# Performance work log

Measured on AMD Instinct MI355X. Metric: run time of the kernel, lower is better.

The kernel has to match this reference:

```python
import jax, jax.numpy as jnp
import numpy as np

EPS = 1e-5
K = 20
NEG_SLOPE = 0.2


def lrelu(x):
    return jnp.where(x >= 0, x, NEG_SLOPE * x)


def bn_train(x, w, b, axes):
    # training-mode batch norm (biased variance), channel axis = 1
    m = jnp.mean(x, axis=axes, keepdims=True)
    v = jnp.mean((x - m) ** 2, axis=axes, keepdims=True)
    shp = [1] * x.ndim
    shp[1] = -1
    return (x - m) * jax.lax.rsqrt(v + EPS) * w.reshape(shp) + b.reshape(shp)


def knn_idx(x, k):
    # x: [B, C, N] -> idx [B, N, k] of k nearest neighbors (max of -dist^2)
    inner = -2.0 * jnp.einsum('bcn,bcm->bnm', x, x)
    xx = jnp.sum(x * x, axis=1)  # [B, N]
    pd = -xx[:, None, :] - inner - xx[:, :, None]  # [B, N, N]
    return jax.lax.top_k(pd, k)[1]


def graph_feature(x, k):
    # x: [B, C, N] -> [B, 2C, N, k] = cat(neighbor - center, center)
    B = x.shape[0]
    idx = knn_idx(x, k)  # [B, N, k]
    xt = jnp.transpose(x, (0, 2, 1))  # [B, N, C]
    nbr = xt[jnp.arange(B)[:, None, None], idx]  # [B, N, k, C] gather
    ctr = jnp.broadcast_to(xt[:, :, None, :], nbr.shape)
    feat = jnp.concatenate([nbr - ctr, ctr], axis=-1)  # [B, N, k, 2C]
    return jnp.transpose(feat, (0, 3, 1, 2))


def edge_conv(x, w, bw, bb):
    # EdgeConv: graph feature -> 1x1 conv (no bias) -> BN -> LeakyReLU -> max over k
    f = graph_feature(x, K)                      # [B, 2C, N, k]
    y = jnp.einsum('bcnk,oc->bonk', f, w)        # 1x1 conv2d
    y = lrelu(bn_train(y, bw, bb, (0, 2, 3)))
    return jnp.max(y, axis=-1)                   # [B, O, N]


def setup_inputs() -> dict:
    key = jax.random.key(0)
    ks = jax.random.split(key, 12)
    B, N = 8, 1024
    s = 0.05
    inp = {'x': jax.random.normal(ks[0], (B, 3, N), dtype=jnp.float32)}
    inp['c1w'] = jax.random.normal(ks[1], (64, 6), dtype=jnp.float32) * s
    inp['c2w'] = jax.random.normal(ks[2], (64, 128), dtype=jnp.float32) * s
    inp['c3w'] = jax.random.normal(ks[3], (128, 128), dtype=jnp.float32) * s
    inp['c4w'] = jax.random.normal(ks[4], (256, 256), dtype=jnp.float32) * s
    inp['c5w'] = jax.random.normal(ks[5], (1024, 512), dtype=jnp.float32) * s
    for i, c in zip(range(1, 8), [64, 64, 128, 256, 1024, 512, 256]):
        inp[f'b{i}w'] = jnp.ones((c,), dtype=jnp.float32)
        inp[f'b{i}b'] = jnp.zeros((c,), dtype=jnp.float32)
    inp['l1w'] = jax.random.normal(ks[6], (512, 2048), dtype=jnp.float32) * s
    inp['l1b'] = jnp.zeros((512,), dtype=jnp.float32)
    inp['l2w'] = jax.random.normal(ks[7], (256, 512), dtype=jnp.float32) * s
    inp['l2b'] = jnp.zeros((256,), dtype=jnp.float32)
    inp['l3w'] = jax.random.normal(ks[8], (40, 256), dtype=jnp.float32) * s
    inp['l3b'] = jnp.zeros((40,), dtype=jnp.float32)
    return inp


def reference(x, c1w, c2w, c3w, c4w, c5w,
              b1w, b1b, b2w, b2b, b3w, b3b, b4w, b4b, b5w, b5b,
              b6w, b6b, b7w, b7b,
              l1w, l1b, l2w, l2b, l3w, l3b):
    x1 = edge_conv(x, c1w, b1w, b1b)    # [B, 64, N]
    x2 = edge_conv(x1, c2w, b2w, b2b)   # [B, 64, N]
    x3 = edge_conv(x2, c3w, b3w, b3b)   # [B, 128, N]
    x4 = edge_conv(x3, c4w, b4w, b4b)   # [B, 256, N]
    cat = jnp.concatenate([x1, x2, x3, x4], axis=1)  # [B, 512, N]
    y = jnp.einsum('bcn,oc->bon', cat, c5w)          # conv5 (1x1)
    y = lrelu(bn_train(y, b5w, b5b, (0, 2)))         # [B, 1024, N]
    feat = jnp.concatenate([jnp.max(y, axis=-1), jnp.mean(y, axis=-1)], axis=1)  # [B, 2048]
    h = feat @ l1w.T + l1b
    h = lrelu(bn_train(h, b6w, b6b, (0,)))
    h = h @ l2w.T + l2b
    h = lrelu(bn_train(h, b7w, b7b, (0,)))
    return h @ l3w.T + l3b  # [B, num_class]
```

## Files before the change

### kernel.cpp

```cpp
#include <hip/hip_runtime.h>
#include <math.h>

#define NPTS 1024
#define NBATCH 8
#define KNN 20
#define KC 24
#define EPSBN 1e-5f
#define NSLOPE 0.2f

typedef __attribute__((ext_vector_type(8))) short short8_t;
typedef __attribute__((ext_vector_type(4))) float floatx4;

__device__ __forceinline__ float lrelu_f(float x){ return x >= 0.f ? x : NSLOPE*x; }

__device__ __forceinline__ unsigned short f2bf_rne(float f){
  union { float f; unsigned u; } x; x.f = f;
  unsigned r = x.u + 0x7FFFu + ((x.u >> 16) & 1u);
  return (unsigned short)(r >> 16);
}
__device__ __forceinline__ float bf2f(unsigned short h){
  union { float f; unsigned u; } x; x.u = ((unsigned)h) << 16;
  return x.f;
}

__global__ void xsplit_t(const float* __restrict__ X, long bstride, int coff, int C, int Cp,
                         unsigned short* __restrict__ Sh, unsigned short* __restrict__ Sl){
  __shared__ float tile[32][33];
  int b = blockIdx.z;
  int c0 = blockIdx.y * 32;
  int n0 = blockIdx.x * 32;
  int t = threadIdx.x;
  int r = t >> 3, q = t & 7;
  float4 rv = make_float4(0,0,0,0);
  if (c0 + r < C)
    rv = *(const float4*)(X + (size_t)b*bstride + (size_t)(coff+c0+r)*NPTS + n0 + q*4);
  tile[r][q*4+0] = rv.x; tile[r][q*4+1] = rv.y; tile[r][q*4+2] = rv.z; tile[r][q*4+3] = rv.w;
  __syncthreads();
  ushort4 oh, ol;
  float f0 = tile[q*4+0][r], f1 = tile[q*4+1][r], f2 = tile[q*4+2][r], f3 = tile[q*4+3][r];
  oh.x = f2bf_rne(f0); ol.x = f2bf_rne(f0 - bf2f(oh.x));
  oh.y = f2bf_rne(f1); ol.y = f2bf_rne(f1 - bf2f(oh.y));
  oh.z = f2bf_rne(f2); ol.z = f2bf_rne(f2 - bf2f(oh.z));
  oh.w = f2bf_rne(f3); ol.w = f2bf_rne(f3 - bf2f(oh.w));
  size_t ob = ((size_t)b*NPTS + n0 + r)*Cp + c0 + q*4;
  *(ushort4*)(Sh + ob) = oh;
  *(ushort4*)(Sl + ob) = ol;
}

__global__ void xx32(const float* __restrict__ X, long bstride, int coff, int C,
                     float* __restrict__ XX){
  int g = blockIdx.x*blockDim.x + threadIdx.x;
  int n = g & (NPTS-1);
  int b = g >> 10;
  const float* p = X + (size_t)b*bstride + (size_t)coff*NPTS + n;
  float s = 0.f;
  for (int c = 0; c < C; ++c){ float v = p[(size_t)c*NPTS]; s += v*v; }
  XX[g] = s;
}

#define LROW 40
__global__ __launch_bounds__(256) void pd_mfma(
    const unsigned short* __restrict__ Sh, const unsigned short* __restrict__ Sl,
    int Cp, const float* __restrict__ XX, float* __restrict__ PD){
  __shared__ __align__(16) unsigned short Ah[128*LROW];
  __shared__ __align__(16) unsigned short Al[128*LROW];
  __shared__ __align__(16) unsigned short Bh[128*LROW];
  __shared__ __align__(16) unsigned short Bl[128*LROW];
  int b  = blockIdx.z;
  int n0 = blockIdx.x * 128;
  int m0 = blockIdx.y * 128;
  int t = threadIdx.x;
  int lane = t & 63, wid = t >> 6;
  int wm = (wid & 1) * 64;
  int wn = (wid >> 1) * 64;
  int fr = lane & 15;
  int fq = (lane >> 4) * 8;
  floatx4 acc[4][4];
  #pragma unroll
  for (int i = 0; i < 4; ++i)
    #pragma unroll
    for (int j = 0; j < 4; ++j) acc[i][j] = (floatx4)(0.f);

  for (int k0 = 0; k0 < Cp; k0 += 32){
    #pragma unroll
    for (int c = 0; c < 2; ++c){
      int ch = t + 256*c;
      int row = ch >> 2, part = (ch & 3)*8;
      size_t ga = ((size_t)b*NPTS + m0 + row)*Cp + k0 + part;
      size_t gb = ((size_t)b*NPTS + n0 + row)*Cp + k0 + part;
      *(short8_t*)&Ah[row*LROW + part] = *(const short8_t*)&Sh[ga];
      *(short8_t*)&Al[row*LROW + part] = *(const short8_t*)&Sl[ga];
      *(short8_t*)&Bh[row*LROW + part] = *(const short8_t*)&Sh[gb];
      *(short8_t*)&Bl[row*LROW + part] = *(const short8_t*)&Sl[gb];
    }
    __syncthreads();
    short8_t afh[4], afl[4], bfh[4], bfl[4];
    #pragma unroll
    for (int mi = 0; mi < 4; ++mi){
      int r = (wm + mi*16 + fr)*LROW + fq;
      afh[mi] = *(const short8_t*)&Ah[r];
      afl[mi] = *(const short8_t*)&Al[r];
    }
    #pragma unroll
    for (int ni = 0; ni < 4; ++ni){
      int r = (wn + ni*16 + fr)*LROW + fq;
      bfh[ni] = *(const short8_t*)&Bh[r];
      bfl[ni] = *(const short8_t*)&Bl[r];
    }
    #pragma unroll
    for (int mi = 0; mi < 4; ++mi)
      #pragma unroll
      for (int ni = 0; ni < 4; ++ni){
        acc[mi][ni] = __builtin_amdgcn_mfma_f32_16x16x32_bf16(afh[mi], bfh[ni], acc[mi][ni], 0, 0, 0);
        acc[mi][ni] = __builtin_amdgcn_mfma_f32_16x16x32_bf16(afl[mi], bfh[ni], acc[mi][ni], 0, 0, 0);
        acc[mi][ni] = __builtin_amdgcn_mfma_f32_16x16x32_bf16(afh[mi], bfl[ni], acc[mi][ni], 0, 0, 0);
      }
    __syncthreads();
  }
  int col = lane & 15;
  int rquad = (lane >> 4) * 4;
  #pragma unroll
  for (int mi = 0; mi < 4; ++mi)
    #pragma unroll
    for (int ni = 0; ni < 4; ++ni){
      int n = n0 + wn + ni*16 + col;
      int mbase = m0 + wm + mi*16 + rquad;
      float4 xx4 = *(const float4*)(XX + (size_t)b*NPTS + mbase);
      floatx4 a = acc[mi][ni];
      float4 o = make_float4(2.f*a.x - xx4.x, 2.f*a.y - xx4.y,
                             2.f*a.z - xx4.z, 2.f*a.w - xx4.w);
      *(float4*)(PD + ((size_t)b*NPTS + n)*NPTS + mbase) = o;
    }
}

__global__ void xt_kernel(const float* __restrict__ X, long bstride, int coff, int C,
                          float* __restrict__ XT){
  __shared__ float tile[32][33];
  int b = blockIdx.z;
  int c0 = blockIdx.y * 32;
  int n0 = blockIdx.x * 32;
  int t = threadIdx.x;
  int r = t >> 3, q = t & 7;
  float4 rv = *(const float4*)(X + (size_t)b*bstride + (size_t)(coff+c0+r)*NPTS + n0 + q*4);
  tile[r][q*4+0] = rv.x; tile[r][q*4+1] = rv.y; tile[r][q*4+2] = rv.z; tile[r][q*4+3] = rv.w;
  __syncthreads();
  float4 ov = make_float4(tile[q*4+0][r], tile[q*4+1][r], tile[q*4+2][r], tile[q*4+3][r]);
  *(float4*)(XT + ((size_t)b*NPTS + n0 + r)*C + c0 + q*4) = ov;
}

__global__ __launch_bounds__(256) void topk_refine(const float* __restrict__ PD,
                                                   const float* __restrict__ X, long bstride,
                                                   int coff, int C,
                                                   const float* __restrict__ XT,
                                                   int* __restrict__ IDX){
  int wid = threadIdx.x >> 6;
  int lane = threadIdx.x & 63;
  int row = blockIdx.x*4 + wid;
  int b = row >> 10, n = row & 1023;
  const float* p = PD + (size_t)row*NPTS;
  unsigned key[16];
  #pragma unroll
  for (int j4 = 0; j4 < 4; ++j4){
    float4 t4 = *(const float4*)&p[lane*16 + j4*4];
    float tv[4] = {t4.x, t4.y, t4.z, t4.w};
    #pragma unroll
    for (int e = 0; e < 4; ++e){
      int j = j4*4 + e;
      unsigned u = __float_as_uint(tv[e]);
      unsigned msk = (unsigned)(((int)u) >> 31) | 0x80000000u;
      key[j] = ((u ^ msk) & 0xFFFFFFF0u) | (unsigned)j;
    }
  }
  #pragma unroll
  for (int ksz = 2; ksz <= 16; ksz <<= 1){
    #pragma unroll
    for (int jj = ksz >> 1; jj > 0; jj >>= 1){
      #pragma unroll
      for (int i = 0; i < 16; ++i){
        int l = i ^ jj;
        if (l > i){
          unsigned a = key[i], c = key[l];
          unsigned mx = a > c ? a : c, mn = a > c ? c : a;
          bool maxfirst = ((i & ksz) == 0);
          key[i] = maxfirst ? mx : mn;
          key[l] = maxfirst ? mn : mx;
        }
      }
    }
  }
  int my_m = 0;
  #pragma unroll
  for (int k = 0; k < KC; ++k){
    unsigned h = key[0];
    unsigned gm = h;
    #pragma unroll
    for (int m = 1; m < 64; m <<= 1){
      unsigned o = (unsigned)__shfl_xor((int)gm, m, 64);
      gm = (o > gm) ? o : gm;
    }
    unsigned long long ball = __ballot(h == gm);
    int wl = __ffsll((unsigned long long)ball) - 1;
    if (lane == k) my_m = wl*16 + (int)(gm & 15u);
    bool isw = (lane == wl);
    #pragma unroll
    for (int i2 = 0; i2 < 15; ++i2) key[i2] = isw ? key[i2+1] : key[i2];
    key[15] = isw ? 0u : key[15];
  }
  double pdv = -1e300; int midx = (1 << 20) + lane;
  if (lane < KC){
    midx = my_m;
    double dot = 0.0, m2 = 0.0, n2 = 0.0;
    if (C == 3){
      const float* Xb = X + (size_t)b*bstride + (size_t)coff*NPTS;
      #pragma unroll
      for (int c = 0; c < 3; ++c){
        double xn = (double)Xb[(size_t)c*NPTS + n];
        double xm = (double)Xb[(size_t)c*NPTS + my_m];
        dot += xn*xm; m2 += xm*xm; n2 += xn*xn;
      }
    } else {
      const float* rn = XT + ((size_t)b*NPTS + n)*C;
      const float* rm = XT + ((size_t)b*NPTS + my_m)*C;
      for (int c = 0; c < C; c += 4){
        float4 xn4 = *(const float4*)&rn[c];
        float4 xm4 = *(const float4*)&rm[c];
        dot += (double)xn4.x*(double)xm4.x + (double)xn4.y*(double)xm4.y
             + (double)xn4.z*(double)xm4.z + (double)xn4.w*(double)xm4.w;
        m2  += (double)xm4.x*(double)xm4.x + (double)xm4.y*(double)xm4.y
             + (double)xm4.z*(double)xm4.z + (double)xm4.w*(double)xm4.w;
        n2  += (double)xn4.x*(double)xn4.x + (double)xn4.y*(double)xn4.y
             + (double)xn4.z*(double)xn4.z + (double)xn4.w*(double)xn4.w;
      }
    }
    pdv = (2.0*dot - m2) - n2;
  }
  int rank = 0;
  #pragma unroll
  for (int j = 0; j < KC; ++j){
    double ov = __shfl(pdv, j, 64);
    int    oi = __shfl(midx, j, 64);
    rank += (ov > pdv || (ov == pdv && oi < midx)) ? 1 : 0;
  }
  if (lane < KC && rank < KNN) IDX[(size_t)row*KNN + rank] = midx;
}

__global__ __launch_bounds__(256) void lin_gemm64(const float* __restrict__ W, int M, int Cdim,
                                                  int lda, int O,
                                                  const float* __restrict__ X, long bstride,
                                                  int coff, float* __restrict__ OUT){
  __shared__ float As[16][68];
  __shared__ float Bs[16][68];
  int b = blockIdx.z;
  int m0 = blockIdx.y * 64;
  int n0 = blockIdx.x * 64;
  int t = threadIdx.x;
  const float* Xb = X + (size_t)b*bstride + (size_t)coff*NPTS;
  float acc[4][4] = {};
  int lr = t >> 4, lc = (t & 15) << 2;
  int tr = (t >> 4) << 2, tc = (t & 15) << 2;
  for (int k0 = 0; k0 < Cdim; k0 += 16){
    int c = k0 + lr;
    float4 av = make_float4(0,0,0,0);
    if (c < Cdim){
      #pragma unroll
      for (int j = 0; j < 4; ++j){
        int m = m0 + lc + j;
        float aval = (m < O) ? W[(size_t)m*lda + c]
                             : W[(size_t)(m-O)*lda + Cdim + c] - W[(size_t)(m-O)*lda + c];
        ((float*)&av)[j] = aval;
      }
    }
    float4 bv = make_float4(0,0,0,0);
    if (c < Cdim)
      bv = *(const float4*)(Xb + (size_t)c*NPTS + n0 + lc);
    *(float4*)&As[lr][lc] = av;
    *(float4*)&Bs[lr][lc] = bv;
    __syncthreads();
    #pragma unroll
    for (int kk = 0; kk < 16; ++kk){
      float4 a4 = *(const float4*)&As[kk][tr];
      float4 b4 = *(const float4*)&Bs[kk][tc];
      float a[4] = {a4.x,a4.y,a4.z,a4.w};
      float bb[4] = {b4.x,b4.y,b4.z,b4.w};
      #pragma unroll
      for (int i = 0; i < 4; ++i)
        #pragma unroll
        for (int j = 0; j < 4; ++j) acc[i][j] += a[i]*bb[j];
    }
    __syncthreads();
  }
  #pragma unroll
  for (int i = 0; i < 4; ++i){
    int m = m0 + tr + i;
    *(float4*)(OUT + ((size_t)b*M + m)*NPTS + n0 + tc) =
        make_float4(acc[i][0],acc[i][1],acc[i][2],acc[i][3]);
  }
}

__global__ void edge_stats(const float* __restrict__ V, const int* __restrict__ IDX, int O,
                           float* __restrict__ YMX, float* __restrict__ YMN,
                           float* __restrict__ S1P, float* __restrict__ S2P){
  __shared__ float vrow[NPTS];
  __shared__ float urow[NPTS];
  __shared__ float r1[256];
  __shared__ float r2[256];
  int b = blockIdx.x / O;
  int o = blockIdx.x % O;
  int t = threadIdx.x;
  const float* vp = V + ((size_t)b*2*O + o)*NPTS;
  const float* up = V + ((size_t)b*2*O + O + o)*NPTS;
  for (int i = 0; i < 4; ++i){ vrow[t+256*i] = vp[t+256*i]; urow[t+256*i] = up[t+256*i]; }
  __syncthreads();
  float s1 = 0.f, s2 = 0.f;
  size_t obase = ((size_t)b*O + o)*NPTS;
  for (int i = 0; i < 4; ++i){
    int n = t + 256*i;
    float un = urow[n];
    const int* ip = IDX + ((size_t)b*NPTS + n)*KNN;
    float mx = -1e38f, mn = 1e38f;
    #pragma unroll
    for (int k = 0; k < KNN; ++k){
      float val = un + vrow[ip[k]];
      mx = fmaxf(mx, val); mn = fminf(mn, val);
      s1 += val; s2 += val*val;
    }
    YMX[obase + n] = mx;
    YMN[obase + n] = mn;
  }
  r1[t] = s1; r2[t] = s2;
  __syncthreads();
  for (int s = 128; s > 0; s >>= 1){
    if (t < s){ r1[t] += r1[t+s]; r2[t] += r2[t+s]; }
    __syncthreads();
  }
  if (t == 0){ S1P[b*O + o] = r1[0]; S2P[b*O + o] = r2[0]; }
}

__global__ void edge_apply(const float* __restrict__ YMX, const float* __restrict__ YMN,
                           const float* __restrict__ S1P, const float* __restrict__ S2P,
                           const float* __restrict__ gw, const float* __restrict__ gb,
                           int O, float* __restrict__ CAT, int coff_out){
  int g = blockIdx.x*blockDim.x + threadIdx.x;
  int n = g & (NPTS-1);
  int o = (g >> 10) % O;
  int b = (g >> 10) / O;
  float s1 = 0.f, s2 = 0.f;
  #pragma unroll
  for (int i = 0; i < NBATCH; ++i){ s1 += S1P[i*O + o]; s2 += S2P[i*O + o]; }
  const float cnt = (float)(NBATCH*NPTS*KNN);
  float mean = s1 / cnt;
  float var = fmaxf(s2 / cnt - mean*mean, 0.f);
  float sc = gw[o] * rsqrtf(var + EPSBN);
  float sh = gb[o] - mean*sc;
  float v = (sc >= 0.f) ? YMX[g] : YMN[g];
  CAT[((size_t)b*512 + coff_out + o)*NPTS + n] = lrelu_f(sc*v + sh);
}

__global__ void wsplit(const float* __restrict__ W, int nelem,
                       unsigned short* __restrict__ Wh, unsigned short* __restrict__ Wl){
  int i = blockIdx.x*blockDim.x + threadIdx.x;
  if (i >= nelem) return;
  float f = W[i];
  unsigned short hi = f2bf_rne(f);
  Wh[i] = hi;
  Wl[i] = f2bf_rne(f - bf2f(hi));
}

__global__ void catsplit_t(const float* __restrict__ CAT,
                           unsigned short* __restrict__ Th, unsigned short* __restrict__ Tl){
  __shared__ float tile[32][33];
  int b = blockIdx.z;
  int c0 = blockIdx.y * 32;
  int n0 = blockIdx.x * 32;
  int t = threadIdx.x;
  int r = t >> 3, q = t & 7;
  float4 rv = *(const float4*)(CAT + ((size_t)b*512 + c0 + r)*NPTS + n0 + q*4);
  tile[r][q*4+0] = rv.x; tile[r][q*4+1] = rv.y; tile[r][q*4+2] = rv.z; tile[r][q*4+3] = rv.w;
  __syncthreads();
  ushort4 oh, ol;
  float f0 = tile[q*4+0][r], f1 = tile[q*4+1][r], f2 = tile[q*4+2][r], f3 = tile[q*4+3][r];
  oh.x = f2bf_rne(f0); ol.x = f2bf_rne(f0 - bf2f(oh.x));
  oh.y = f2bf_rne(f1); ol.y = f2bf_rne(f1 - bf2f(oh.y));
  oh.z = f2bf_rne(f2); ol.z = f2bf_rne(f2 - bf2f(oh.z));
  oh.w = f2bf_rne(f3); ol.w = f2bf_rne(f3 - bf2f(oh.w));
  size_t ob = ((size_t)b*NPTS + n0 + r)*512 + c0 + q*4;
  *(ushort4*)(Th + ob) = oh;
  *(ushort4*)(Tl + ob) = ol;
}

__global__ __launch_bounds__(256) void conv5_mfma(
    const unsigned short* __restrict__ Ath, const unsigned short* __restrict__ Atl,
    const unsigned short* __restrict__ Wh,  const unsigned short* __restrict__ Wl,
    float* __restrict__ OUT){
  __shared__ __align__(16) unsigned short Ah[128*LROW];
  __shared__ __align__(16) unsigned short Al[128*LROW];
  __shared__ __align__(16) unsigned short Bh[128*LROW];
  __shared__ __align__(16) unsigned short Bl[128*LROW];
  int b  = blockIdx.z;
  int n0 = blockIdx.x * 128;
  int m0 = blockIdx.y * 128;
  int t = threadIdx.x;
  int lane = t & 63, wid = t >> 6;
  int wn = (wid & 1) * 64;
  int wm = (wid >> 1) * 64;
  int fr = lane & 15;
  int fq = (lane >> 4) * 8;
  floatx4 acc[4][4];
  #pragma unroll
  for (int i = 0; i < 4; ++i)
    #pragma unroll
    for (int j = 0; j < 4; ++j) acc[i][j] = (floatx4)(0.f);

  for (int k0 = 0; k0 < 512; k0 += 32){
    #pragma unroll
    for (int c = 0; c < 2; ++c){
      int ch = t + 256*c;
      int row = ch >> 2, part = (ch & 3)*8;
      size_t ga = ((size_t)b*NPTS + n0 + row)*512 + k0 + part;
      size_t gb = ((size_t)(m0 + row))*512 + k0 + part;
      *(short8_t*)&Ah[row*LROW + part] = *(const short8_t*)&Ath[ga];
      *(short8_t*)&Al[row*LROW + part] = *(const short8_t*)&Atl[ga];
      *(short8_t*)&Bh[row*LROW + part] = *(const short8_t*)&Wh[gb];
      *(short8_t*)&Bl[row*LROW + part] = *(const short8_t*)&Wl[gb];
    }
    __syncthreads();
    short8_t afh[4], afl[4], bfh[4], bfl[4];
    #pragma unroll
    for (int ni = 0; ni < 4; ++ni){
      int r = (wn + ni*16 + fr)*LROW + fq;
      afh[ni] = *(const short8_t*)&Ah[r];
      afl[ni] = *(const short8_t*)&Al[r];
    }
    #pragma unroll
    for (int mi = 0; mi < 4; ++mi){
      int r = (wm + mi*16 + fr)*LROW + fq;
      bfh[mi] = *(const short8_t*)&Bh[r];
      bfl[mi] = *(const short8_t*)&Bl[r];
    }
    #pragma unroll
    for (int ni = 0; ni < 4; ++ni)
      #pragma unroll
      for (int mi = 0; mi < 4; ++mi){
        acc[ni][mi] = __builtin_amdgcn_mfma_f32_16x16x32_bf16(afh[ni], bfh[mi], acc[ni][mi], 0, 0, 0);
        acc[ni][mi] = __builtin_amdgcn_mfma_f32_16x16x32_bf16(afl[ni], bfh[mi], acc[ni][mi], 0, 0, 0);
        acc[ni][mi] = __builtin_amdgcn_mfma_f32_16x16x32_bf16(afh[ni], bfl[mi], acc[ni][mi], 0, 0, 0);
      }
    __syncthreads();
  }
  int col = lane & 15;
  int rquad = (lane >> 4) * 4;
  #pragma unroll
  for (int ni = 0; ni < 4; ++ni)
    #pragma unroll
    for (int mi = 0; mi < 4; ++mi){
      int m = m0 + wm + mi*16 + col;
      int n = n0 + wn + ni*16 + rquad;
      *(floatx4*)(OUT + ((size_t)b*1024 + m)*NPTS + n) = acc[ni][mi];
    }
}

__global__ void y5_stats(const float* __restrict__ Y5, float* __restrict__ S1, float* __restrict__ S2){
  __shared__ float r1[256], r2[256];
  int o = blockIdx.x;
  int t = threadIdx.x;
  float s1 = 0.f, s2 = 0.f;
  for (int b = 0; b < NBATCH; ++b){
    const float* p = Y5 + ((size_t)b*1024 + o)*NPTS;
    for (int n = t; n < NPTS; n += 256){ float v = p[n]; s1 += v; s2 += v*v; }
  }
  r1[t] = s1; r2[t] = s2;
  __syncthreads();
  for (int s = 128; s > 0; s >>= 1){
    if (t < s){ r1[t] += r1[t+s]; r2[t] += r2[t+s]; }
    __syncthreads();
  }
  if (t == 0){ S1[o] = r1[0]; S2[o] = r2[0]; }
}

__global__ void head_kernel(const float* __restrict__ Y5, const float* __restrict__ S1,
                            const float* __restrict__ S2,
                            const float* __restrict__ gw, const float* __restrict__ gb,
                            float* __restrict__ FEAT){
  __shared__ float rm[256], rs[256];
  int o = blockIdx.x & 1023;
  int b = blockIdx.x >> 10;
  int t = threadIdx.x;
  const float cnt = (float)(NBATCH*NPTS);
  float mean = S1[o] / cnt;
  float var = fmaxf(S2[o] / cnt - mean*mean, 0.f);
  float s = gw[o] * rsqrtf(var + EPSBN);
  float sh = gb[o] - mean*s;
  const float* p = Y5 + ((size_t)b*1024 + o)*NPTS;
  float mx = -1e38f, sm = 0.f;
  for (int n = t; n < NPTS; n += 256){
    float v = lrelu_f(s*p[n] + sh);
    mx = fmaxf(mx, v); sm += v;
  }
  rm[t] = mx; rs[t] = sm;
  __syncthreads();
  for (int st = 128; st > 0; st >>= 1){
    if (t < st){ rm[t] = fmaxf(rm[t], rm[t+st]); rs[t] += rs[t+st]; }
    __syncthreads();
  }
  if (t == 0){
    FEAT[(size_t)b*2048 + o]        = rm[0];
    FEAT[(size_t)b*2048 + 1024 + o] = rs[0] * (1.f/NPTS);
  }
}

__global__ void fc_bn(const float* __restrict__ IN, int ID, int OD,
                      const float* __restrict__ W, const float* __restrict__ bias,
                      const float* __restrict__ gw, const float* __restrict__ gb,
                      float* __restrict__ OUT){
  __shared__ float red[256][8];
  int f = blockIdx.x;
  int t = threadIdx.x;
  float acc[8] = {};
  const float* wr = W + (size_t)f*ID;
  for (int j = t; j < ID; j += 256){
    float wv = wr[j];
    #pragma unroll
    for (int b = 0; b < 8; ++b) acc[b] += IN[b*ID + j] * wv;
  }
  #pragma unroll
  for (int b = 0; b < 8; ++b) red[t][b] = acc[b];
  __syncthreads();
  for (int s = 128; s > 0; s >>= 1){
    if (t < s){
      #pragma unroll
      for (int b = 0; b < 8; ++b) red[t][b] += red[t+s][b];
    }
    __syncthreads();
  }
  if (t == 0){
    float h[8], mean = 0.f;
    #pragma unroll
    for (int b = 0; b < 8; ++b){ h[b] = red[0][b] + bias[f]; mean += h[b]; }
    mean *= 0.125f;
    float var = 0.f;
    #pragma unroll
    for (int b = 0; b < 8; ++b){ float d = h[b]-mean; var += d*d; }
    var *= 0.125f;
    float sc = gw[f]*rsqrtf(var + EPSBN);
    float sh = gb[f] - mean*sc;
    #pragma unroll
    for (int b = 0; b < 8; ++b) OUT[b*OD + f] = lrelu_f(sc*h[b] + sh);
  }
}

__global__ void fc_out(const float* __restrict__ IN, const float* __restrict__ W,
                       const float* __restrict__ bias, float* __restrict__ OUT){
  __shared__ float red[256][8];
  int j = blockIdx.x;
  int t = threadIdx.x;
  float wv = W[(size_t)j*256 + t];
  #pragma unroll
  for (int b = 0; b < 8; ++b) red[t][b] = IN[b*256 + t] * wv;
  __syncthreads();
  for (int s = 128; s > 0; s >>= 1){
    if (t < s){
      #pragma unroll
      for (int b = 0; b < 8; ++b) red[t][b] += red[t+s][b];
    }
    __syncthreads();
  }
  if (t == 0){
    #pragma unroll
    for (int b = 0; b < 8; ++b) OUT[b*40 + j] = red[0][b] + bias[j];
  }
}

extern "C" void kernel_launch(void* const* d_in, const int* in_sizes, int n_in,
                              void* d_out, int out_size, void* d_ws, size_t ws_size,
                              hipStream_t stream) {
  const float* x   = (const float*)d_in[0];
  const float* cw[5] = { (const float*)d_in[1], (const float*)d_in[2], (const float*)d_in[3],
                         (const float*)d_in[4], (const float*)d_in[5] };
  const float* bw[7]; const float* bbv[7];
  for (int i = 0; i < 7; ++i){ bw[i] = (const float*)d_in[6+2*i]; bbv[i] = (const float*)d_in[7+2*i]; }
  const float* l1w = (const float*)d_in[20]; const float* l1b = (const float*)d_in[21];
  const float* l2w = (const float*)d_in[22]; const float* l2b = (const float*)d_in[23];
  const float* l3w = (const float*)d_in[24]; const float* l3b = (const float*)d_in[25];
  float* out = (float*)d_out;

  float* ws = (float*)d_ws;
  float* PD    = ws;
  float* V     = ws;
  float* YMX   = ws + 4194304;
  float* YMN   = ws + 6291456;
  float* Y5    = ws;
  float* XT    = ws + 8388608;
  unsigned short* XSH = (unsigned short*)(ws + 9437184);
  unsigned short* XSL = (unsigned short*)(ws + 9961472);
  float* XX    = ws + 10485760;
  unsigned short* CATth = (unsigned short*)(ws + 8388608);
  unsigned short* CATtl = (unsigned short*)(ws + 10485760);
  unsigned short* WhP   = (unsigned short*)(ws + 12582912);
  unsigned short* WlP   = (unsigned short*)(ws + 12845056);
  float* CAT   = ws + 16777216;
  int*   IDX   = (int*)(ws + 20987904);
  float* S1P   = ws + 21151744;
  float* S2P   = ws + 21159936;
  float* FEAT  = ws + 21170176;
  float* H1    = ws + 21186560;
  float* H2    = ws + 21190656;

  struct L { int C, Cp, O; const float* in; long bs; int ci; const float* w; int bn; int co; };
  L ls[4] = {
    { 3,   32,  64, x,   (long)3*NPTS,   0,   cw[0], 0, 0   },
    { 64,  64,  64, CAT, (long)512*NPTS, 0,   cw[1], 1, 64  },
    { 64,  64, 128, CAT, (long)512*NPTS, 64,  cw[2], 2, 128 },
    { 128, 128,256, CAT, (long)512*NPTS, 128, cw[3], 3, 256 },
  };

  for (int li = 0; li < 4; ++li){
    L& l = ls[li];
    xsplit_t<<<dim3(32, l.Cp/32, NBATCH), 256, 0, stream>>>(l.in, l.bs, l.ci, l.C, l.Cp, XSH, XSL);
    xx32<<<(NBATCH*NPTS)/256, 256, 0, stream>>>(l.in, l.bs, l.ci, l.C, XX);
    pd_mfma<<<dim3(8,8,NBATCH), 256, 0, stream>>>(XSH, XSL, l.Cp, XX, PD);
    if (l.C >= 32)
      xt_kernel<<<dim3(32, l.C/32, NBATCH), 256, 0, stream>>>(l.in, l.bs, l.ci, l.C, XT);
    topk_refine<<<(NBATCH*NPTS)/4, 256, 0, stream>>>(PD, l.in, l.bs, l.ci, l.C, XT, IDX);
    lin_gemm64<<<dim3(16, (2*l.O)/64, NBATCH), 256, 0, stream>>>(
        l.w, 2*l.O, l.C, 2*l.C, l.O, l.in, l.bs, l.ci, V);
    edge_stats<<<NBATCH*l.O, 256, 0, stream>>>(V, IDX, l.O, YMX, YMN, S1P, S2P);
    edge_apply<<<(NBATCH*l.O*NPTS)/256, 256, 0, stream>>>(
        YMX, YMN, S1P, S2P, bw[l.bn], bbv[l.bn], l.O, CAT, l.co);
  }

  wsplit<<<(1024*512+255)/256, 256, 0, stream>>>(cw[4], 1024*512, WhP, WlP);
  catsplit_t<<<dim3(32,16,NBATCH), 256, 0, stream>>>(CAT, CATth, CATtl);
  conv5_mfma<<<dim3(8,8,NBATCH), 256, 0, stream>>>(CATth, CATtl, WhP, WlP, Y5);

  y5_stats<<<1024, 256, 0, stream>>>(Y5, S1P, S2P);
  head_kernel<<<NBATCH*1024, 256, 0, stream>>>(Y5, S1P, S2P, bw[4], bbv[4], FEAT);

  fc_bn<<<512, 256, 0, stream>>>(FEAT, 2048, 512, l1w, l1b, bw[5], bbv[5], H1);
  fc_bn<<<256, 256, 0, stream>>>(H1, 512, 256, l2w, l2b, bw[6], bbv[6], H2);
  fc_out<<<40, 256, 0, stream>>>(H2, l3w, l3b, out);
}
```

Baseline: 571.3 us.

## Fuse split/norm/transpose prep kernels and process two rows per wave in top-k

Merges the bf16 hi/lo split, squared-norm, and fp32 transpose kernels into one prep kernel that loads each 32-point column tile into shared memory once. This cuts two launches per layer and avoids re-reading the input three times. Separately, top-k now handles two PD rows per wavefront, interleaving the two sorts and shuffle reductions for more instruction-level parallelism and half the blocks. The cost is higher register pressure in top-k and a prep grid of only 256 blocks of 256 threads, with a shared tile of up to 128 channel rows.

```diff
diff --git a/kernel.cpp b/kernel.cpp
--- a/kernel.cpp
+++ b/kernel.cpp
@@ -23,39 +23,53 @@
   return x.f;
 }
 
-__global__ void xsplit_t(const float* __restrict__ X, long bstride, int coff, int C, int Cp,
-                         unsigned short* __restrict__ Sh, unsigned short* __restrict__ Sl){
-  __shared__ float tile[32][33];
-  int b = blockIdx.z;
-  int c0 = blockIdx.y * 32;
+__global__ __launch_bounds__(256) void prep(const float* __restrict__ X, long bstride, int coff,
+                                            int C, int Cp,
+                                            unsigned short* __restrict__ Sh,
+                                            unsigned short* __restrict__ Sl,
+                                            float* __restrict__ XT, float* __restrict__ XX){
+  __shared__ float tile[128][33];
+  __shared__ float part[32][8];
+  int b = blockIdx.y;
   int n0 = blockIdx.x * 32;
   int t = threadIdx.x;
   int r = t >> 3, q = t & 7;
-  float4 rv = make_float4(0,0,0,0);
-  if (c0 + r < C)
-    rv = *(const float4*)(X + (size_t)b*bstride + (size_t)(coff+c0+r)*NPTS + n0 + q*4);
-  tile[r][q*4+0] = rv.x; tile[r][q*4+1] = rv.y; tile[r][q*4+2] = rv.z; tile[r][q*4+3] = rv.w;
-  __syncthreads();
-  ushort4 oh, ol;
-  float f0 = tile[q*4+0][r], f1 = tile[q*4+1][r], f2 = tile[q*4+2][r], f3 = tile[q*4+3][r];
-  oh.x = f2bf_rne(f0); ol.x = f2bf_rne(f0 - bf2f(oh.x));
-  oh.y = f2bf_rne(f1); ol.y = f2bf_rne(f1 - bf2f(oh.y));
-  oh.z = f2bf_rne(f2); ol.z = f2bf_rne(f2 - bf2f(oh.z));
-  oh.w = f2bf_rne(f3); ol.w = f2bf_rne(f3 - bf2f(oh.w));
-  size_t ob = ((size_t)b*NPTS + n0 + r)*Cp + c0 + q*4;
-  *(ushort4*)(Sh + ob) = oh;
-  *(ushort4*)(Sl + ob) = ol;
-}
-
-__global__ void xx32(const float* __restrict__ X, long bstride, int coff, int C,
-                     float* __restrict__ XX){
-  int g = blockIdx.x*blockDim.x + threadIdx.x;
-  int n = g & (NPTS-1);
-  int b = g >> 10;
-  const float* p = X + (size_t)b*bstride + (size_t)coff*NPTS + n;
+  for (int c0 = 0; c0 < C; c0 += 32){
+    int row = c0 + r;
+    if (row < C){
+      float4 rv = *(const float4*)(X + (size_t)b*bstride + (size_t)(coff+row)*NPTS + n0 + q*4);
+      tile[row][q*4+0] = rv.x; tile[row][q*4+1] = rv.y;
+      tile[row][q*4+2] = rv.z; tile[row][q*4+3] = rv.w;
+    }
+  }
+  __syncthreads();
+  size_t bn = (size_t)b*NPTS + n0 + r;
+  for (int c0 = 0; c0 < Cp; c0 += 32){
+    int c = c0 + q*4;
+    float f0 = (c+0 < C) ? tile[c+0][r] : 0.f;
+    float f1 = (c+1 < C) ? tile[c+1][r] : 0.f;
+    float f2 = (c+2 < C) ? tile[c+2][r] : 0.f;
+    float f3 = (c+3 < C) ? tile[c+3][r] : 0.f;
+    if (C >= 32 && c < C)
+      *(float4*)(XT + bn*C + c) = make_float4(f0,f1,f2,f3);
+    ushort4 oh, ol;
+    oh.x = f2bf_rne(f0); ol.x = f2bf_rne(f0 - bf2f(oh.x));
+    oh.y = f2bf_rne(f1); ol.y = f2bf_rne(f1 - bf2f(oh.y));
+    oh.z = f2bf_rne(f2); ol.z = f2bf_rne(f2 - bf2f(oh.z));
+    oh.w = f2bf_rne(f3); ol.w = f2bf_rne(f3 - bf2f(oh.w));
+    *(ushort4*)(Sh + bn*Cp + c) = oh;
+    *(ushort4*)(Sl + bn*Cp + c) = ol;
+  }
   float s = 0.f;
-  for (int c = 0; c < C; ++c){ float v = p[(size_t)c*NPTS]; s += v*v; }
-  XX[g] = s;
+  for (int c = q; c < C; c += 8){ float v = tile[c][r]; s += v*v; }
+  part[r][q] = s;
+  __syncthreads();
+  if (q == 0){
+    float s8 = 0.f;
+    #pragma unroll
+    for (int i = 0; i < 8; ++i) s8 += part[r][i];
+    XX[(size_t)b*NPTS + n0 + r] = s8;
+  }
 }
 
 #define LROW 40
@@ -133,21 +147,6 @@
     }
 }
 
-__global__ void xt_kernel(const float* __restrict__ X, long bstride, int coff, int C,
-                          float* __restrict__ XT){
-  __shared__ float tile[32][33];
-  int b = blockIdx.z;
-  int c0 = blockIdx.y * 32;
-  int n0 = blockIdx.x * 32;
-  int t = threadIdx.x;
-  int r = t >> 3, q = t & 7;
-  float4 rv = *(const float4*)(X + (size_t)b*bstride + (size_t)(coff+c0+r)*NPTS + n0 + q*4);
-  tile[r][q*4+0] = rv.x; tile[r][q*4+1] = rv.y; tile[r][q*4+2] = rv.z; tile[r][q*4+3] = rv.w;
-  __syncthreads();
-  float4 ov = make_float4(tile[q*4+0][r], tile[q*4+1][r], tile[q*4+2][r], tile[q*4+3][r]);
-  *(float4*)(XT + ((size_t)b*NPTS + n0 + r)*C + c0 + q*4) = ov;
-}
-
 __global__ __launch_bounds__(256) void topk_refine(const float* __restrict__ PD,
                                                    const float* __restrict__ X, long bstride,
                                                    int coff, int C,
@@ -155,20 +154,28 @@
                                                    int* __restrict__ IDX){
   int wid = threadIdx.x >> 6;
   int lane = threadIdx.x & 63;
-  int row = blockIdx.x*4 + wid;
-  int b = row >> 10, n = row & 1023;
-  const float* p = PD + (size_t)row*NPTS;
-  unsigned key[16];
+  int rowA = blockIdx.x*8 + wid*2;
+  int rowB = rowA + 1;
+  int b = rowA >> 10;
+  int nA = rowA & 1023, nB = rowB & 1023;
+  const float* pA = PD + (size_t)rowA*NPTS;
+  const float* pB = PD + (size_t)rowB*NPTS;
+  unsigned keyA[16], keyB[16];
   #pragma unroll
   for (int j4 = 0; j4 < 4; ++j4){
-    float4 t4 = *(const float4*)&p[lane*16 + j4*4];
-    float tv[4] = {t4.x, t4.y, t4.z, t4.w};
+    float4 a4 = *(const float4*)&pA[lane*16 + j4*4];
+    float4 b4 = *(const float4*)&pB[lane*16 + j4*4];
+    float av[4] = {a4.x,a4.y,a4.z,a4.w};
+    float bv[4] = {b4.x,b4.y,b4.z,b4.w};
     #pragma unroll
     for (int e = 0; e < 4; ++e){
       int j = j4*4 + e;
-      unsigned u = __float_as_uint(tv[e]);
-      unsigned msk = (unsigned)(((int)u) >> 31) | 0x80000000u;
-      key[j] = ((u ^ msk) & 0xFFFFFFF0u) | (unsigned)j;
+      unsigned ua = __float_as_uint(av[e]);
+      unsigned ma = (unsigned)(((int)ua) >> 31) | 0x80000000u;
+      keyA[j] = ((ua ^ ma) & 0xFFFFFFF0u) | (unsigned)j;
+      unsigned ub = __float_as_uint(bv[e]);
+      unsigned mb = (unsigned)(((int)ub) >> 31) | 0x80000000u;
+      keyB[j] = ((ub ^ mb) & 0xFFFFFFF0u) | (unsigned)j;
     }
   }
   #pragma unroll
@@ -179,35 +186,51 @@
       for (int i = 0; i < 16; ++i){
         int l = i ^ jj;
         if (l > i){
-          unsigned a = key[i], c = key[l];
+          bool maxfirst = ((i & ksz) == 0);
+          unsigned a = keyA[i], c = keyA[l];
           unsigned mx = a > c ? a : c, mn = a > c ? c : a;
-          bool maxfirst = ((i & ksz) == 0);
-          key[i] = maxfirst ? mx : mn;
-          key[l] = maxfirst ? mn : mx;
+          keyA[i] = maxfirst ? mx : mn; keyA[l] = maxfirst ? mn : mx;
+          unsigned a2 = keyB[i], c2 = keyB[l];
+          unsigned mx2 = a2 > c2 ? a2 : c2, mn2 = a2 > c2 ? c2 : a2;
+          keyB[i] = maxfirst ? mx2 : mn2; keyB[l] = maxfirst ? mn2 : mx2;
         }
       }
     }
   }
-  int my_m = 0;
+  int my_mA = 0, my_mB = 0;
   #pragma unroll
   for (int k = 0; k < KC; ++k){
-    unsigned h = key[0];
-    unsigned gm = h;
+    unsigned hA = keyA[0], hB = keyB[0];
+    unsigned gA = hA, gB = hB;
     #pragma unroll
     for (int m = 1; m < 64; m <<= 1){
-      unsigned o = (unsigned)__shfl_xor((int)gm, m, 64);
-      gm = (o > gm) ? o : gm;
-    }
-    unsigned long long ball = __ballot(h == gm);
-    int wl = __ffsll((unsigned long long)ball) - 1;
-    if (lane == k) my_m = wl*16 + (int)(gm & 15u);
-    bool isw = (lane == wl);
-    #pragma unroll
-    for (int i2 = 0; i2 < 15; ++i2) key[i2] = isw ? key[i2+1] : key[i2];
-    key[15] = isw ? 0u : key[15];
-  }
+      unsigned oA = (unsigned)__shfl_xor((int)gA, m, 64);
+      unsigned oB = (unsigned)__shfl_xor((int)gB, m, 64);
+      gA = (oA > gA) ? oA : gA;
+      gB = (oB > gB) ? oB : gB;
+    }
+    unsigned long long ballA = __ballot(hA == gA);
+    unsigned long long ballB = __ballot(hB == gB);
+    int wlA = __ffsll(ballA) - 1;
+    int wlB = __ffsll(ballB) - 1;
+    if (lane == k)      my_mA = wlA*16 + (int)(gA & 15u);
+    if (lane == 32 + k) my_mB = wlB*16 + (int)(gB & 15u);
+    bool iwA = (lane == wlA), iwB = (lane == wlB);
+    #pragma unroll
+    for (int i2 = 0; i2 < 15; ++i2){
+      keyA[i2] = iwA ? keyA[i2+1] : keyA[i2];
+      keyB[i2] = iwB ? keyB[i2+1] : keyB[i2];
+    }
+    keyA[15] = iwA ? 0u : keyA[15];
+    keyB[15] = iwB ? 0u : keyB[15];
+  }
+  bool grpB = lane >= 32;
+  int lk = grpB ? lane - 32 : lane;
+  int row = grpB ? rowB : rowA;
+  int n = grpB ? nB : nA;
+  int my_m = grpB ? my_mB : my_mA;
   double pdv = -1e300; int midx = (1 << 20) + lane;
-  if (lane < KC){
+  if (lk < KC){
     midx = my_m;
     double dot = 0.0, m2 = 0.0, n2 = 0.0;
     if (C == 3){
@@ -234,14 +257,15 @@
     }
     pdv = (2.0*dot - m2) - n2;
   }
+  int base = grpB ? 32 : 0;
   int rank = 0;
   #pragma unroll
   for (int j = 0; j < KC; ++j){
-    double ov = __shfl(pdv, j, 64);
-    int    oi = __shfl(midx, j, 64);
+    double ov = __shfl(pdv, base + j, 64);
+    int    oi = __shfl(midx, base + j, 64);
     rank += (ov > pdv || (ov == pdv && oi < midx)) ? 1 : 0;
   }
-  if (lane < KC && rank < KNN) IDX[(size_t)row*KNN + rank] = midx;
+  if (lk < KC && rank < KNN) IDX[(size_t)row*KNN + rank] = midx;
 }
 
 __global__ __launch_bounds__(256) void lin_gemm64(const float* __restrict__ W, int M, int Cdim,
@@ -615,12 +639,9 @@
 
   for (int li = 0; li < 4; ++li){
     L& l = ls[li];
-    xsplit_t<<<dim3(32, l.Cp/32, NBATCH), 256, 0, stream>>>(l.in, l.bs, l.ci, l.C, l.Cp, XSH, XSL);
-    xx32<<<(NBATCH*NPTS)/256, 256, 0, stream>>>(l.in, l.bs, l.ci, l.C, XX);
+    prep<<<dim3(32, NBATCH), 256, 0, stream>>>(l.in, l.bs, l.ci, l.C, l.Cp, XSH, XSL, XT, XX);
     pd_mfma<<<dim3(8,8,NBATCH), 256, 0, stream>>>(XSH, XSL, l.Cp, XX, PD);
-    if (l.C >= 32)
-      xt_kernel<<<dim3(32, l.C/32, NBATCH), 256, 0, stream>>>(l.in, l.bs, l.ci, l.C, XT);
-    topk_refine<<<(NBATCH*NPTS)/4, 256, 0, stream>>>(PD, l.in, l.bs, l.ci, l.C, XT, IDX);
+    topk_refine<<<(NBATCH*NPTS)/8, 256, 0, stream>>>(PD, l.in, l.bs, l.ci, l.C, XT, IDX);
     lin_gemm64<<<dim3(16, (2*l.O)/64, NBATCH), 256, 0, stream>>>(
         l.w, 2*l.O, l.C, 2*l.C, l.O, l.in, l.bs, l.ci, V);
     edge_stats<<<NBATCH*l.O, 256, 0, stream>>>(V, IDX, l.O, YMX, YMN, S1P, S2P);
```

Measured after the change: 505.1 us. 11.6% less time.
